# Performance work log

Measured on AMD Instinct MI355X. Metric: run time of the kernel, lower is better.

The kernel has to match this reference:

```python
import jax, jax.numpy as jnp
import numpy as np

KS = 3          # kernel_size
NUM_FA = 16     # number of functional atoms per pixel
TOTAL_BASES = 6 # num_bases * (ks // 2)
BN_EPS = 1e-5


def _conv3x3(x, w, b):
    # NCHW conv, padding=1, stride=1
    y = jax.lax.conv_general_dilated(
        x, w, window_strides=(1, 1), padding=[(1, 1), (1, 1)],
        dimension_numbers=("NCHW", "OIHW", "NCHW"))
    return y + b[None, :, None, None]


def _bn(x, gamma, beta, mean, var):
    scale = gamma / jnp.sqrt(var + BN_EPS)
    return (x - mean[None, :, None, None]) * scale[None, :, None, None] + beta[None, :, None, None]


def setup_inputs() -> dict:
    key = jax.random.key(0)
    ks = jax.random.split(key, 16)
    N, C, H, W = 16, 64, 64, 64
    INTER, BC_DIM, O = 64, TOTAL_BASES * NUM_FA, 128
    f32 = jnp.float32
    return {
        "x": jax.random.normal(ks[0], (N, C, H, W), f32),
        "conv1_w": jax.random.normal(ks[1], (INTER, C, 3, 3), f32) * 0.05,
        "conv1_b": jax.random.normal(ks[2], (INTER,), f32) * 0.05,
        "bn1_gamma": jax.random.uniform(ks[3], (INTER,), f32, 0.5, 1.5),
        "bn1_beta": jax.random.normal(ks[4], (INTER,), f32) * 0.05,
        "bn1_mean": jax.random.normal(ks[5], (INTER,), f32) * 0.05,
        "bn1_var": jax.random.uniform(ks[6], (INTER,), f32, 0.5, 1.5),
        "conv2_w": jax.random.normal(ks[7], (BC_DIM, INTER, 3, 3), f32) * 0.05,
        "conv2_b": jax.random.normal(ks[8], (BC_DIM,), f32) * 0.05,
        "bn2_gamma": jax.random.uniform(ks[9], (BC_DIM,), f32, 0.5, 1.5),
        "bn2_beta": jax.random.normal(ks[10], (BC_DIM,), f32) * 0.05,
        "bn2_mean": jax.random.normal(ks[11], (BC_DIM,), f32) * 0.05,
        "bn2_var": jax.random.uniform(ks[12], (BC_DIM,), f32, 0.5, 1.5),
        "bases": jax.random.normal(ks[13], (TOTAL_BASES, KS * KS), f32),
        "coef": jax.random.normal(ks[14], (O, C * NUM_FA), f32) * 0.02,
    }


def reference(x, conv1_w, conv1_b, bn1_gamma, bn1_beta, bn1_mean, bn1_var,
              conv2_w, conv2_b, bn2_gamma, bn2_beta, bn2_mean, bn2_var,
              bases, coef):
    N, C, H, W = x.shape
    # bases_net: conv3x3 -> BN -> tanh -> conv3x3 -> BN -> tanh
    h = jnp.tanh(_bn(_conv3x3(x, conv1_w, conv1_b), bn1_gamma, bn1_beta, bn1_mean, bn1_var))
    bc = jnp.tanh(_bn(_conv3x3(h, conv2_w, conv2_b), bn2_gamma, bn2_beta, bn2_mean, bn2_var))
    # torch: .transpose(1,-1).view(N,H,W,num_fa,total_bases)  (swaps H/W; H==W)
    bases_coef = jnp.transpose(bc, (0, 3, 2, 1)).reshape(N, H, W, NUM_FA, TOTAL_BASES)
    # atoms: (bases_coef[...,None] * bases).sum(-2).transpose(-1,-2) -> (N,H,W,ks2,num_fa)
    atoms = jnp.einsum("nhwft,tk->nhwkf", bases_coef, bases)
    # unfold(x, ks, padding=1) -> patches (N,H,W,C,ks2), channel-major like torch unfold
    xp = jnp.pad(x, ((0, 0), (0, 0), (1, 1), (1, 1)))
    patches = jnp.stack([xp[:, :, i:i + H, j:j + W] for i in range(KS) for j in range(KS)], axis=2)  # (N,C,9,H,W)
    patches = jnp.transpose(patches, (0, 3, 4, 1, 2))  # (N,H,W,C,9)
    # (x.unsqueeze(-1) * atoms.unsqueeze(-3)).sum(-2) -> (N,H,W,C,num_fa) -> flatten C-major
    bases_out = jnp.einsum("nhwck,nhwkf->nhwcf", patches, atoms).reshape(N, H, W, C * NUM_FA)
    # torch: .transpose(1,-1) -> (N, C*num_fa, W, H), then 1x1 conv with coef
    out = jnp.einsum("nhwd,od->nowh", bases_out, coef)  # (N, O, W, H)
    return out
```

## Files before the change

kernel.cpp:

```cpp
#include <hip/hip_runtime.h>
#include <math.h>
#include <string.h>

#define NBATCH 16

typedef __attribute__((ext_vector_type(8))) short short8;
typedef __attribute__((ext_vector_type(4))) float floatx4;
typedef __fp16 half2v __attribute__((ext_vector_type(2)));
#define MFMA16(a, b, c) __builtin_amdgcn_mfma_f32_16x16x32_bf16(a, b, c, 0, 0, 0)

__device__ __forceinline__ unsigned int cvtpk(float a, float b) {
  unsigned int r;
  asm("v_cvt_pk_bf16_f32 %0, %1, %2" : "=v"(r) : "v"(a), "v"(b));
  return r;
}
__device__ __forceinline__ unsigned short f2bf(float f) {
  return (unsigned short)(cvtpk(f, 0.f) & 0xffffu);
}
__device__ __forceinline__ unsigned int packbf2(float a, float b) {
  return cvtpk(a, b);
}
__device__ __forceinline__ float bflo(unsigned int u) {
  return __uint_as_float(u << 16);
}
__device__ __forceinline__ float bfhi(unsigned int u) {
  return __uint_as_float(u & 0xffff0000u);
}
__device__ __forceinline__ float fast_tanh(float x) {
  float e = __expf(2.f * x);
  return 1.f - 2.f / (e + 1.f);
}

__global__ void prep_weights(const float* __restrict__ w1,
                             const float* __restrict__ w2,
                             const float* __restrict__ coef,
                             unsigned short* __restrict__ w1swz,
                             unsigned short* __restrict__ w2swz,
                             unsigned short* __restrict__ coefswz) {
  int i = blockIdx.x * 256 + threadIdx.x;
  if (i < 131072) {
    int j = i & 7, f = i >> 3;
    int lane = f & 63;
    int u = (f >> 6) & 3;
    int wj = (f >> 8) & 1;
    int kc = (f >> 9) & 1;
    int rd = f >> 10;
    int lm = lane & 15, lq = lane >> 4;
    int oc = wj * 64 + u * 16 + lm;
    int k = rd * 64 + kc * 32 + lq * 8 + j;
    coefswz[i] = f2bf(coef[oc * 1024 + k]);
  }
  if (i < 36864) {
    int j = i & 7, f = i >> 3;
    int lane = f & 63;
    int u = (f >> 6) & 1;
    int wn = (f >> 7) & 1;
    int kc = (f >> 8) & 1;
    int off = f >> 9;
    int lm = lane & 15, lq = lane >> 4;
    int oc = wn * 32 + u * 16 + lm;
    int ic = kc * 32 + lq * 8 + j;
    w1swz[i] = f2bf(w1[(oc * 64 + ic) * 9 + off]);
  }
  if (i < 55296) {
    int j = i & 7, f = i >> 3;
    int lane = f & 63;
    int rem = f >> 6;
    int u = rem % 3;
    int rem2 = rem / 3;
    int wn = rem2 & 1;
    int kc = (rem2 >> 1) & 1;
    int off = rem2 >> 2;
    int lm = lane & 15, lq = lane >> 4;
    int oc = wn * 48 + u * 16 + lm;
    int ic = kc * 32 + lq * 8 + j;
    w2swz[i] = f2bf(w2[(oc * 64 + ic) * 9 + off]);
  }
}

__global__ __launch_bounds__(256) void xb_prep(const float* __restrict__ x,
                                               unsigned short* __restrict__ xb) {
  __shared__ float tile[64][65];
  const int t = threadIdx.x;
  const int y = blockIdx.x, n = blockIdx.y;
  const float* xn = x + (size_t)n * 64 * 4096 + y * 64;
#pragma unroll
  for (int it = 0; it < 16; ++it) {
    int idx = it * 256 + t;
    int c = idx >> 6, xx = idx & 63;
    tile[c][xx] = xn[c * 4096 + xx];
  }
  __syncthreads();
  const int xx = t >> 2, cq = t & 3;
  unsigned short* dst = xb + ((size_t)n * 4096 + y * 64 + xx) * 64;
#pragma unroll
  for (int jj = 0; jj < 2; ++jj) {
    int ch0 = cq * 16 + jj * 8;
    unsigned int p[4];
#pragma unroll
    for (int e = 0; e < 4; ++e)
      p[e] = packbf2(tile[ch0 + e * 2][xx], tile[ch0 + e * 2 + 1][xx]);
    *(uint4*)&dst[ch0] = make_uint4(p[0], p[1], p[2], p[3]);
  }
}

__global__ __launch_bounds__(256) void fused_conv(
    const unsigned short* __restrict__ xb, const unsigned short* __restrict__ w1swz,
    const unsigned short* __restrict__ w2swz, const float* __restrict__ b1,
    const float* __restrict__ g1, const float* __restrict__ be1,
    const float* __restrict__ m1, const float* __restrict__ v1,
    const float* __restrict__ b2, const float* __restrict__ g2,
    const float* __restrict__ be2, const float* __restrict__ m2,
    const float* __restrict__ v2, unsigned short* __restrict__ bcg) {
  __shared__ unsigned short xls[144 * 72];
  __shared__ unsigned short hls[128 * 72];

  const int t = threadIdx.x;
  const int tile = blockIdx.x, n = blockIdx.y;
  const int x0 = (tile & 7) * 8, y0 = (tile >> 3) * 8;

  const unsigned short* xbn = xb + (size_t)n * 4096 * 64;
#pragma unroll
  for (int it = 0; it < 5; ++it) {
    int idx = it * 256 + t;
    if (idx < 1152) {
      int pos = idx >> 3, u4 = idx & 7;
      int xr = pos / 12, xc = pos - xr * 12;
      int gy = y0 - 2 + xr, gx = x0 - 2 + xc;
      uint4 v = {0u, 0u, 0u, 0u};
      if ((unsigned)gy < 64u && (unsigned)gx < 64u)
        v = *(const uint4*)&xbn[((size_t)gy * 64 + gx) * 64 + u4 * 8];
      *(uint4*)&xls[pos * 72 + u4 * 8] = v;
    }
  }
  __syncthreads();

  const int lane = t & 63, w = t >> 6;
  const int wm = w & 1, wn = w >> 1;
  const int lm = lane & 15, lq = lane >> 4;

  int abase[4];
#pragma unroll
  for (int i = 0; i < 4; ++i) {
    int px = (wm + 2 * i) * 16 + lm;
    if (px > 99) px = 99;
    int hr = px / 10, hc = px - hr * 10;
    abase[i] = (hr * 12 + hc) * 72 + lq * 8;
  }
  floatx4 acc[4][2];
#pragma unroll
  for (int i = 0; i < 4; ++i)
#pragma unroll
    for (int u = 0; u < 2; ++u) acc[i][u] = floatx4{0.f, 0.f, 0.f, 0.f};

#pragma unroll
  for (int step = 0; step < 18; ++step) {
    const int off = step >> 1, kc = step & 1;
    const int di = off / 3, dj = off % 3;
    short8 b[2];
#pragma unroll
    for (int u = 0; u < 2; ++u)
      b[u] = *(const short8*)&w1swz[(off * 512 + kc * 256 + wn * 128 + u * 64 +
                                     lane) * 8];
#pragma unroll
    for (int i = 0; i < 4; ++i) {
      short8 a = *(const short8*)&xls[abase[i] + (di * 12 + dj) * 72 + kc * 32];
      acc[i][0] = MFMA16(a, b[0], acc[i][0]);
      acc[i][1] = MFMA16(a, b[1], acc[i][1]);
    }
  }
  {
    float sc[2], sh[2];
#pragma unroll
    for (int u = 0; u < 2; ++u) {
      int oc = wn * 32 + u * 16 + lm;
      sc[u] = g1[oc] * rsqrtf(v1[oc] + 1e-5f);
      sh[u] = (b1[oc] - m1[oc]) * sc[u] + be1[oc];
    }
#pragma unroll
    for (int i = 0; i < 4; ++i) {
      int px0 = (wm + 2 * i) * 16 + lq * 4;
#pragma unroll
      for (int u = 0; u < 2; ++u) {
        int oc = wn * 32 + u * 16 + lm;
#pragma unroll
        for (int r = 0; r < 4; ++r) {
          int px = px0 + r;
          if (px < 100) {
            int hr = px / 10, hc = px - hr * 10;
            int gy = y0 - 1 + hr, gx = x0 - 1 + hc;
            bool valid = ((unsigned)gy < 64u) && ((unsigned)gx < 64u);
            float val = valid ? fast_tanh(acc[i][u][r] * sc[u] + sh[u]) : 0.f;
            hls[px * 72 + oc] = f2bf(val);
          }
        }
      }
    }
  }
  __syncthreads();

  int hbase[2];
#pragma unroll
  for (int s = 0; s < 2; ++s) {
    int opx = (wm + 2 * s) * 16 + lm;
    int yl = opx >> 3, xl = opx & 7;
    hbase[s] = (yl * 10 + xl) * 72 + lq * 8;
  }
  floatx4 acc2[2][3];
#pragma unroll
  for (int s = 0; s < 2; ++s)
#pragma unroll
    for (int u = 0; u < 3; ++u) acc2[s][u] = floatx4{0.f, 0.f, 0.f, 0.f};

#pragma unroll
  for (int step = 0; step < 18; ++step) {
    const int off = step >> 1, kc = step & 1;
    const int di = off / 3, dj = off % 3;
    short8 b[3];
#pragma unroll
    for (int u = 0; u < 3; ++u)
      b[u] = *(const short8*)&w2swz[(off * 768 + kc * 384 + wn * 192 + u * 64 +
                                     lane) * 8];
#pragma unroll
    for (int s = 0; s < 2; ++s) {
      short8 a = *(const short8*)&hls[hbase[s] + (di * 10 + dj) * 72 + kc * 32];
      acc2[s][0] = MFMA16(a, b[0], acc2[s][0]);
      acc2[s][1] = MFMA16(a, b[1], acc2[s][1]);
      acc2[s][2] = MFMA16(a, b[2], acc2[s][2]);
    }
  }
  {
    float sc[3], sh[3];
#pragma unroll
    for (int u = 0; u < 3; ++u) {
      int oc = wn * 48 + u * 16 + lm;
      sc[u] = g2[oc] * rsqrtf(v2[oc] + 1e-5f);
      sh[u] = (b2[oc] - m2[oc]) * sc[u] + be2[oc];
    }
    unsigned short* bcn = bcg + (size_t)n * 4096 * 96;
#pragma unroll
    for (int s = 0; s < 2; ++s) {
      int opx0 = (wm + 2 * s) * 16 + lq * 4;
#pragma unroll
      for (int u = 0; u < 3; ++u) {
        int oc = wn * 48 + u * 16 + lm;
#pragma unroll
        for (int r = 0; r < 4; ++r) {
          int opx = opx0 + r;
          int y = y0 + (opx >> 3), xx = x0 + (opx & 7);
          bcn[((size_t)y * 64 + xx) * 96 + oc] =
              f2bf(fast_tanh(acc2[s][u][r] * sc[u] + sh[u]));
        }
      }
    }
  }
}

__global__ __launch_bounds__(256, 2) void adconv_final(
    const unsigned short* __restrict__ xb, const unsigned short* __restrict__ bc,
    const float* __restrict__ bases, const unsigned short* __restrict__ coefswz,
    float* __restrict__ out) {
  __shared__ unsigned short xs[100 * 72];
  __shared__ unsigned short As[4 * 1024];

  const int t = threadIdx.x;
  const int tile = blockIdx.x, n = blockIdx.y;
  const int q0 = (tile & 7) * 8, p0 = (tile >> 3) * 8;

  float bs[54];
#pragma unroll
  for (int i = 0; i < 54; ++i) bs[i] = bases[i];

  const unsigned short* xbn = xb + (size_t)n * 4096 * 64;
#pragma unroll
  for (int it = 0; it < 4; ++it) {
    int idx = it * 256 + t;
    if (idx < 800) {
      int pos = idx >> 3, u4 = idx & 7;
      int row = pos / 10, col = pos - row * 10;
      int gp = p0 - 1 + row, gq = q0 - 1 + col;
      uint4 v = {0u, 0u, 0u, 0u};
      if ((unsigned)gp < 64u && (unsigned)gq < 64u)
        v = *(const uint4*)&xbn[((size_t)gp * 64 + gq) * 64 + u4 * 8];
      *(uint4*)&xs[pos * 72 + u4 * 8] = v;
    }
  }

  const int lane = t & 63, w = t >> 6;
  const int lm = lane & 15, lq = lane >> 4;

  const int pxl_b = lane >> 2, fh4 = lane & 3;
  const int px_b = w * 16 + pxl_b;
  const int qx_b = px_b >> 3, py_b = px_b & 7;

  float atf[9][4];
  {
    const unsigned short* bp =
        bc + ((size_t)n * 4096 + (q0 + qx_b) * 64 + (p0 + py_b)) * 96 + fh4 * 24;
    float bcv[24];
#pragma unroll
    for (int m = 0; m < 3; ++m) {
      uint4 v = *(const uint4*)(bp + m * 8);
      unsigned int uu[4] = {v.x, v.y, v.z, v.w};
#pragma unroll
      for (int e = 0; e < 4; ++e) {
        bcv[m * 8 + e * 2] = bflo(uu[e]);
        bcv[m * 8 + e * 2 + 1] = bfhi(uu[e]);
      }
    }
#pragma unroll
    for (int j = 0; j < 4; ++j)
#pragma unroll
      for (int k = 0; k < 9; ++k) {
        float s0 = 0.f;
#pragma unroll
        for (int tt = 0; tt < 6; ++tt)
          s0 = fmaf(bcv[j * 6 + tt], bs[tt * 9 + k], s0);
        atf[k][j] = s0;
      }
  }

  int pa[9];
#pragma unroll
  for (int i = 0; i < 3; ++i)
#pragma unroll
    for (int j = 0; j < 3; ++j)
      pa[i * 3 + j] = ((py_b + i) * 10 + qx_b + j) * 72;

  floatx4 acc[2][4];
#pragma unroll
  for (int wj = 0; wj < 2; ++wj)
#pragma unroll
    for (int u = 0; u < 4; ++u) acc[wj][u] = floatx4{0.f, 0.f, 0.f, 0.f};

  unsigned short* Asw = &As[w * 1024];

  uint2 qv[9];
  auto qload = [&](int rd) {
    const int coff = rd * 4;
#pragma unroll
    for (int p = 0; p < 9; ++p) qv[p] = *(const uint2*)&xs[pa[p] + coff];
  };
  auto build = [&]() {
    float a[4][4];
    {
      float c0 = bflo(qv[0].x), c1 = bfhi(qv[0].x);
      float c2 = bflo(qv[0].y), c3 = bfhi(qv[0].y);
#pragma unroll
      for (int j = 0; j < 4; ++j) {
        float av = atf[0][j];
        a[0][j] = c0 * av;
        a[1][j] = c1 * av;
        a[2][j] = c2 * av;
        a[3][j] = c3 * av;
      }
    }
#pragma unroll
    for (int p = 1; p < 9; ++p) {
      float c0 = bflo(qv[p].x), c1 = bfhi(qv[p].x);
      float c2 = bflo(qv[p].y), c3 = bfhi(qv[p].y);
#pragma unroll
      for (int j = 0; j < 4; ++j) {
        float av = atf[p][j];
        a[0][j] = fmaf(c0, av, a[0][j]);
        a[1][j] = fmaf(c1, av, a[1][j]);
        a[2][j] = fmaf(c2, av, a[2][j]);
        a[3][j] = fmaf(c3, av, a[3][j]);
      }
    }
#pragma unroll
    for (int cc = 0; cc < 4; ++cc) {
      int g = (cc * 4 + fh4) ^ ((pxl_b & 7) << 1);
      uint2 val;
      val.x = cvtpk(a[cc][0], a[cc][1]);
      val.y = cvtpk(a[cc][2], a[cc][3]);
      *(uint2*)&Asw[pxl_b * 64 + g * 4] = val;
    }
  };

  __syncthreads();
  qload(0);
  build();

  for (int rd = 0; rd < 16; ++rd) {
    short8 Bf[2][2][4];
#pragma unroll
    for (int kc = 0; kc < 2; ++kc)
#pragma unroll
      for (int wj = 0; wj < 2; ++wj)
#pragma unroll
        for (int u = 0; u < 4; ++u) {
          int frag = ((rd * 2 + kc) * 2 + wj) * 4 + u;
          Bf[kc][wj][u] =
              *(const short8*)(coefswz + ((size_t)frag * 64 + lane) * 8);
        }
    short8 Af[2];
#pragma unroll
    for (int kc = 0; kc < 2; ++kc) {
      int u16 = (kc * 4 + lq) ^ (lm & 7);
      Af[kc] = *(const short8*)&Asw[lm * 64 + u16 * 8];
    }
    if (rd < 15) {
      qload(rd + 1);
      build();
    }
    __builtin_amdgcn_s_setprio(1);
#pragma unroll
    for (int kc = 0; kc < 2; ++kc)
#pragma unroll
      for (int wj = 0; wj < 2; ++wj)
#pragma unroll
        for (int u = 0; u < 4; ++u)
          acc[wj][u] = MFMA16(Af[kc], Bf[kc][wj][u], acc[wj][u]);
    __builtin_amdgcn_s_setprio(0);
  }

  float* outn = out + (size_t)n * 128 * 4096;
#pragma unroll
  for (int wj = 0; wj < 2; ++wj)
#pragma unroll
    for (int u = 0; u < 4; ++u) {
      int oc = wj * 64 + u * 16 + lm;
      int gpx = w * 16 + lq * 4;
      int qx = gpx >> 3, py0 = gpx & 7;
      *(float4*)&outn[((size_t)oc * 64 + q0 + qx) * 64 + p0 + py0] =
          make_float4(acc[wj][u][0], acc[wj][u][1], acc[wj][u][2],
                      acc[wj][u][3]);
    }
}

extern "C" void kernel_launch(void* const* d_in, const int* in_sizes, int n_in,
                              void* d_out, int out_size, void* d_ws,
                              size_t ws_size, hipStream_t stream) {
  const float* x = (const float*)d_in[0];
  const float* conv1_w = (const float*)d_in[1];
  const float* conv1_b = (const float*)d_in[2];
  const float* bn1_g = (const float*)d_in[3];
  const float* bn1_b = (const float*)d_in[4];
  const float* bn1_m = (const float*)d_in[5];
  const float* bn1_v = (const float*)d_in[6];
  const float* conv2_w = (const float*)d_in[7];
  const float* conv2_b = (const float*)d_in[8];
  const float* bn2_g = (const float*)d_in[9];
  const float* bn2_b = (const float*)d_in[10];
  const float* bn2_m = (const float*)d_in[11];
  const float* bn2_v = (const float*)d_in[12];
  const float* bases = (const float*)d_in[13];
  const float* coef = (const float*)d_in[14];
  float* out = (float*)d_out;

  char* ws = (char*)d_ws;
  unsigned short* xbuf = (unsigned short*)(ws);
  unsigned short* bcb = (unsigned short*)(ws + 8388608);
  unsigned short* w1swz = (unsigned short*)(ws + 20971520);
  unsigned short* w2swz = (unsigned short*)(ws + 21045248);
  unsigned short* coefswz = (unsigned short*)(ws + 21155840);

  prep_weights<<<512, 256, 0, stream>>>(conv1_w, conv2_w, coef, w1swz, w2swz,
                                        coefswz);
  xb_prep<<<dim3(64, NBATCH), 256, 0, stream>>>(x, xbuf);
  fused_conv<<<dim3(64, NBATCH), 256, 0, stream>>>(
      xbuf, w1swz, w2swz, conv1_b, bn1_g, bn1_b, bn1_m, bn1_v, conv2_b, bn2_g,
      bn2_b, bn2_m, bn2_v, bcb);
  adconv_final<<<dim3(64, NBATCH), 256, 0, stream>>>(xbuf, bcb, bases, coefswz,
                                                     out);
}
```

Before: 170.5 us.

## Merge prep kernels into one launch and stage x tile as fp32 in LDS

Combines the weight-swizzle and x-to-bf16 prep kernels into a single launch, using extra blocks for the weight work, to save one kernel launch and its tail. In the final kernel the x halo tile is unpacked from bf16 to fp32 once when it is staged into shared memory, so the inner build loop no longer does bf16 shifts and masks on every reload. It also adds a compiler memory barrier after the coefficient fragment loads to control scheduling. The cost is a larger LDS footprint (about 27KB instead of about 14KB for the x tile), which could limit occupancy under launch_bounds(256,2), plus wider LDS reads per round.

```diff
diff --git a/kernel.cpp b/kernel.cpp
--- a/kernel.cpp
+++ b/kernel.cpp
@@ -6,7 +6,6 @@
 
 typedef __attribute__((ext_vector_type(8))) short short8;
 typedef __attribute__((ext_vector_type(4))) float floatx4;
-typedef __fp16 half2v __attribute__((ext_vector_type(2)));
 #define MFMA16(a, b, c) __builtin_amdgcn_mfma_f32_16x16x32_bf16(a, b, c, 0, 0, 0)
 
 __device__ __forceinline__ unsigned int cvtpk(float a, float b) {
@@ -31,13 +30,37 @@
   return 1.f - 2.f / (e + 1.f);
 }
 
-__global__ void prep_weights(const float* __restrict__ w1,
-                             const float* __restrict__ w2,
-                             const float* __restrict__ coef,
-                             unsigned short* __restrict__ w1swz,
-                             unsigned short* __restrict__ w2swz,
-                             unsigned short* __restrict__ coefswz) {
-  int i = blockIdx.x * 256 + threadIdx.x;
+__global__ __launch_bounds__(256) void prep_all(
+    const float* __restrict__ x, unsigned short* __restrict__ xb,
+    const float* __restrict__ w1, const float* __restrict__ w2,
+    const float* __restrict__ coef, unsigned short* __restrict__ w1swz,
+    unsigned short* __restrict__ w2swz, unsigned short* __restrict__ coefswz) {
+  __shared__ float tile[64][65];
+  const int t = threadIdx.x;
+  if (blockIdx.x < 64) {
+    const int y = blockIdx.x, n = blockIdx.y;
+    const float* xn = x + (size_t)n * 64 * 4096 + y * 64;
+#pragma unroll
+    for (int it = 0; it < 16; ++it) {
+      int idx = it * 256 + t;
+      int c = idx >> 6, xx = idx & 63;
+      tile[c][xx] = xn[c * 4096 + xx];
+    }
+    __syncthreads();
+    const int xx = t >> 2, cq = t & 3;
+    unsigned short* dst = xb + ((size_t)n * 4096 + y * 64 + xx) * 64;
+#pragma unroll
+    for (int jj = 0; jj < 2; ++jj) {
+      int ch0 = cq * 16 + jj * 8;
+      unsigned int p[4];
+#pragma unroll
+      for (int e = 0; e < 4; ++e)
+        p[e] = packbf2(tile[ch0 + e * 2][xx], tile[ch0 + e * 2 + 1][xx]);
+      *(uint4*)&dst[ch0] = make_uint4(p[0], p[1], p[2], p[3]);
+    }
+    return;
+  }
+  int i = ((blockIdx.x - 64) * NBATCH + blockIdx.y) * 256 + t;
   if (i < 131072) {
     int j = i & 7, f = i >> 3;
     int lane = f & 63;
@@ -78,32 +101,6 @@
   }
 }
 
-__global__ __launch_bounds__(256) void xb_prep(const float* __restrict__ x,
-                                               unsigned short* __restrict__ xb) {
-  __shared__ float tile[64][65];
-  const int t = threadIdx.x;
-  const int y = blockIdx.x, n = blockIdx.y;
-  const float* xn = x + (size_t)n * 64 * 4096 + y * 64;
-#pragma unroll
-  for (int it = 0; it < 16; ++it) {
-    int idx = it * 256 + t;
-    int c = idx >> 6, xx = idx & 63;
-    tile[c][xx] = xn[c * 4096 + xx];
-  }
-  __syncthreads();
-  const int xx = t >> 2, cq = t & 3;
-  unsigned short* dst = xb + ((size_t)n * 4096 + y * 64 + xx) * 64;
-#pragma unroll
-  for (int jj = 0; jj < 2; ++jj) {
-    int ch0 = cq * 16 + jj * 8;
-    unsigned int p[4];
-#pragma unroll
-    for (int e = 0; e < 4; ++e)
-      p[e] = packbf2(tile[ch0 + e * 2][xx], tile[ch0 + e * 2 + 1][xx]);
-    *(uint4*)&dst[ch0] = make_uint4(p[0], p[1], p[2], p[3]);
-  }
-}
-
 __global__ __launch_bounds__(256) void fused_conv(
     const unsigned short* __restrict__ xb, const unsigned short* __restrict__ w1swz,
     const unsigned short* __restrict__ w2swz, const float* __restrict__ b1,
@@ -260,7 +257,7 @@
     const unsigned short* __restrict__ xb, const unsigned short* __restrict__ bc,
     const float* __restrict__ bases, const unsigned short* __restrict__ coefswz,
     float* __restrict__ out) {
-  __shared__ unsigned short xs[100 * 72];
+  __shared__ float xs[100 * 68];
   __shared__ unsigned short As[4 * 1024];
 
   const int t = threadIdx.x;
@@ -282,7 +279,10 @@
       uint4 v = {0u, 0u, 0u, 0u};
       if ((unsigned)gp < 64u && (unsigned)gq < 64u)
         v = *(const uint4*)&xbn[((size_t)gp * 64 + gq) * 64 + u4 * 8];
-      *(uint4*)&xs[pos * 72 + u4 * 8] = v;
+      float* d = &xs[pos * 68 + u4 * 8];
+      *(float4*)d = make_float4(bflo(v.x), bfhi(v.x), bflo(v.y), bfhi(v.y));
+      *(float4*)(d + 4) =
+          make_float4(bflo(v.z), bfhi(v.z), bflo(v.w), bfhi(v.w));
     }
   }
 
@@ -325,7 +325,7 @@
   for (int i = 0; i < 3; ++i)
 #pragma unroll
     for (int j = 0; j < 3; ++j)
-      pa[i * 3 + j] = ((py_b + i) * 10 + qx_b + j) * 72;
+      pa[i * 3 + j] = ((py_b + i) * 10 + qx_b + j) * 68;
 
   floatx4 acc[2][4];
 #pragma unroll
@@ -335,37 +335,33 @@
 
   unsigned short* Asw = &As[w * 1024];
 
-  uint2 qv[9];
+  float4 qv[9];
   auto qload = [&](int rd) {
     const int coff = rd * 4;
 #pragma unroll
-    for (int p = 0; p < 9; ++p) qv[p] = *(const uint2*)&xs[pa[p] + coff];
+    for (int p = 0; p < 9; ++p) qv[p] = *(const float4*)&xs[pa[p] + coff];
   };
   auto build = [&]() {
     float a[4][4];
     {
-      float c0 = bflo(qv[0].x), c1 = bfhi(qv[0].x);
-      float c2 = bflo(qv[0].y), c3 = bfhi(qv[0].y);
 #pragma unroll
       for (int j = 0; j < 4; ++j) {
         float av = atf[0][j];
-        a[0][j] = c0 * av;
-        a[1][j] = c1 * av;
-        a[2][j] = c2 * av;
-        a[3][j] = c3 * av;
+        a[0][j] = qv[0].x * av;
+        a[1][j] = qv[0].y * av;
+        a[2][j] = qv[0].z * av;
+        a[3][j] = qv[0].w * av;
       }
     }
 #pragma unroll
     for (int p = 1; p < 9; ++p) {
-      float c0 = bflo(qv[p].x), c1 = bfhi(qv[p].x);
-      float c2 = bflo(qv[p].y), c3 = bfhi(qv[p].y);
 #pragma unroll
       for (int j = 0; j < 4; ++j) {
         float av = atf[p][j];
-        a[0][j] = fmaf(c0, av, a[0][j]);
-        a[1][j] = fmaf(c1, av, a[1][j]);
-        a[2][j] = fmaf(c2, av, a[2][j]);
-        a[3][j] = fmaf(c3, av, a[3][j]);
+        a[0][j] = fmaf(qv[p].x, av, a[0][j]);
+        a[1][j] = fmaf(qv[p].y, av, a[1][j]);
+        a[2][j] = fmaf(qv[p].z, av, a[2][j]);
+        a[3][j] = fmaf(qv[p].w, av, a[3][j]);
       }
     }
 #pragma unroll
@@ -394,6 +390,7 @@
           Bf[kc][wj][u] =
               *(const short8*)(coefswz + ((size_t)frag * 64 + lane) * 8);
         }
+    asm volatile("" ::: "memory");
     short8 Af[2];
 #pragma unroll
     for (int kc = 0; kc < 2; ++kc) {
@@ -456,9 +453,8 @@
   unsigned short* w2swz = (unsigned short*)(ws + 21045248);
   unsigned short* coefswz = (unsigned short*)(ws + 21155840);
 
-  prep_weights<<<512, 256, 0, stream>>>(conv1_w, conv2_w, coef, w1swz, w2swz,
-                                        coefswz);
-  xb_prep<<<dim3(64, NBATCH), 256, 0, stream>>>(x, xbuf);
+  prep_all<<<dim3(96, NBATCH), 256, 0, stream>>>(x, xbuf, conv1_w, conv2_w,
+                                                 coef, w1swz, w2swz, coefswz);
   fused_conv<<<dim3(64, NBATCH), 256, 0, stream>>>(
       xbuf, w1swz, w2swz, conv1_b, bn1_g, bn1_b, bn1_m, bn1_v, conv2_b, bn2_g,
       bn2_b, bn2_m, bn2_v, bcb);
```

Result: faster. 165.7 us (-2.8%).
